# Kernel optimization log

Hardware: AMD Instinct MI355X
Metric: run time of the kernel (lower is better)

## Reference

```python
import jax, jax.numpy as jnp
import numpy as np

H, C = 8, 16           # heads, per-head channels
NEG_SLOPE = 0.2        # PyG GATConv leaky_relu slope
N_NODES, N_EDGES, F_IN, N_GRAPHS = 50000, 600000, 64, 500


def setup_inputs() -> dict:
    key = jax.random.key(0)
    ks = jax.random.split(key, 24)
    s = 0.1  # weight init scale
    inp = {
        "x": jax.random.normal(ks[0], (N_NODES, F_IN), jnp.float32),
        "edge_index": jax.random.randint(ks[1], (2, N_EDGES), 0, N_NODES, dtype=jnp.int64),
        "batch": jnp.sort(jax.random.randint(ks[2], (N_NODES,), 0, N_GRAPHS, dtype=jnp.int64)),
        "W1": jax.random.normal(ks[3], (F_IN, H * C), jnp.float32) * s,
        "as1": jax.random.normal(ks[4], (H, C), jnp.float32) * s,
        "ad1": jax.random.normal(ks[5], (H, C), jnp.float32) * s,
        "b1": jnp.zeros((H * C,), jnp.float32),
        "W2": jax.random.normal(ks[6], (H * C, H * C), jnp.float32) * s,
        "as2": jax.random.normal(ks[7], (H, C), jnp.float32) * s,
        "ad2": jax.random.normal(ks[8], (H, C), jnp.float32) * s,
        "b2": jnp.zeros((H * C,), jnp.float32),
        "W3": jax.random.normal(ks[9], (H * C, H * C), jnp.float32) * s,
        "as3": jax.random.normal(ks[10], (H, C), jnp.float32) * s,
        "ad3": jax.random.normal(ks[11], (H, C), jnp.float32) * s,
        "b3": jnp.zeros((H * C,), jnp.float32),
        "fc1_w": jax.random.normal(ks[12], (H * C, 10), jnp.float32) * s,
        "fc1_b": jnp.zeros((10,), jnp.float32),
        "fc2_w": jax.random.normal(ks[13], (10, 1), jnp.float32) * s,
        "fc2_b": jnp.zeros((1,), jnp.float32),
    }
    return inp


def gat_layer(x, src, dst, W, att_src, att_dst, bias, n):
    # x: [N, F_in] -> h: [N, H, C]
    h = (x @ W).reshape(n, H, C)
    a_src = jnp.sum(h * att_src, axis=-1)  # [N, H]
    a_dst = jnp.sum(h * att_dst, axis=-1)  # [N, H]
    e = jax.nn.leaky_relu(a_src[src] + a_dst[dst], NEG_SLOPE)  # [E, H]
    # per-destination segment softmax (numerically stable)
    m = jax.ops.segment_max(e, dst, num_segments=n)            # [N, H]
    e = jnp.exp(e - m[dst])
    z = jax.ops.segment_sum(e, dst, num_segments=n)            # [N, H]
    alpha = e / (z[dst] + 1e-16)                               # [E, H]
    out = jax.ops.segment_sum(h[src] * alpha[:, :, None], dst, num_segments=n)  # [N, H, C]
    return out.reshape(n, H * C) + bias


def reference(x, edge_index, batch, W1, as1, ad1, b1, W2, as2, ad2, b2,
              W3, as3, ad3, b3, fc1_w, fc1_b, fc2_w, fc2_b):
    n = x.shape[0]
    # PyG GATConv default add_self_loops=True
    loop = jnp.arange(n, dtype=edge_index.dtype)
    src = jnp.concatenate([edge_index[0], loop])
    dst = jnp.concatenate([edge_index[1], loop])

    x = jax.nn.relu(gat_layer(x, src, dst, W1, as1, ad1, b1, n))
    x = jax.nn.relu(gat_layer(x, src, dst, W2, as2, ad2, b2, n))
    x = jax.nn.relu(gat_layer(x, src, dst, W3, as3, ad3, b3, n))

    # global_mean_pool over graphs
    sums = jax.ops.segment_sum(x, batch, num_segments=N_GRAPHS)          # [G, 128]
    cnts = jax.ops.segment_sum(jnp.ones((n,), x.dtype), batch, num_segments=N_GRAPHS)
    pooled = sums / jnp.maximum(cnts, 1.0)[:, None]

    hdn = jax.nn.relu(pooled @ fc1_w + fc1_b)
    return hdn @ fc2_w + fc2_b  # [G, 1]
```

## Files before the change

### kernel.cpp

```cpp
#include <hip/hip_runtime.h>
#include <hip/hip_bf16.h>

#define H 8
#define C 16
#define HC 128
#define NEG_SLOPE 0.2f

__global__ void init_build_kernel(int* __restrict__ zp, int nz,
                                  int* __restrict__ csr, int cap, int sentinel) {
    int i = blockIdx.x * 256 + threadIdx.x;
    if (i < nz) zp[i] = 0;
    if (i < cap) csr[i] = sentinel;
}

__global__ void hist_both_kernel(const int* __restrict__ ei, const int* __restrict__ batch,
                                 int* __restrict__ deg, int* __restrict__ gcnt, int E, int N) {
    int i = blockIdx.x * 256 + threadIdx.x;
    if (i < E + N) {
        int d = (i < E) ? ei[E + i] : i - E;
        atomicAdd(&deg[d], 1);
    }
    if (i < N) atomicAdd(&gcnt[batch[i]], 1);
}

__global__ void scan_blk2_kernel(const int* __restrict__ a1, int* __restrict__ o1,
                                 int* __restrict__ p1, int n1, int nb1, int pad1,
                                 const int* __restrict__ a2, int* __restrict__ o2,
                                 int* __restrict__ p2, int n2, int pad2) {
    __shared__ int sh[256];
    const int* a; int* o; int* p; int n, blk, pad;
    if ((int)blockIdx.x < nb1) { a = a1; o = o1; p = p1; n = n1; blk = blockIdx.x; pad = pad1; }
    else { a = a2; o = o2; p = p2; n = n2; blk = blockIdx.x - nb1; pad = pad2; }
    int tid = threadIdx.x;
    int base = blk * 1024 + tid * 4;
    int4 v = make_int4(0, 0, 0, 0);
    if (base + 3 < n) v = *(const int4*)(a + base);
    else {
        if (base < n)     v.x = a[base];
        if (base + 1 < n) v.y = a[base + 1];
        if (base + 2 < n) v.z = a[base + 2];
        if (base + 3 < n) v.w = a[base + 3];
    }
    if (pad) { v.x = (v.x + 7) & ~7; v.y = (v.y + 7) & ~7; v.z = (v.z + 7) & ~7; v.w = (v.w + 7) & ~7; }
    int s = v.x + v.y + v.z + v.w;
    sh[tid] = s;
    __syncthreads();
    for (int off = 1; off < 256; off <<= 1) {
        int t = (tid >= off) ? sh[tid - off] : 0;
        __syncthreads();
        sh[tid] += t;
        __syncthreads();
    }
    int excl = sh[tid] - s;
    int4 ov;
    ov.x = excl; ov.y = ov.x + v.x; ov.z = ov.y + v.y; ov.w = ov.z + v.z;
    if (base + 3 < n) *(int4*)(o + base) = ov;
    else {
        if (base < n)     o[base] = ov.x;
        if (base + 1 < n) o[base + 1] = ov.y;
        if (base + 2 < n) o[base + 2] = ov.z;
        if (base + 3 < n) o[base + 3] = ov.w;
    }
    if (tid == 255) p[blk] = sh[255];
}

__global__ void scan_part2_kernel(int* __restrict__ p1, int* __restrict__ tot1, int nb1,
                                  int* __restrict__ p2, int* __restrict__ tot2, int nb2) {
    __shared__ int sh[256];
    int tid = threadIdx.x;
    int v = (tid < nb1) ? p1[tid] : 0;
    sh[tid] = v;
    __syncthreads();
    for (int off = 1; off < 256; off <<= 1) {
        int t = (tid >= off) ? sh[tid - off] : 0;
        __syncthreads();
        sh[tid] += t;
        __syncthreads();
    }
    if (tid < nb1) p1[tid] = sh[tid] - v;
    if (tid == 255) *tot1 = sh[255];
    __syncthreads();
    v = (tid < nb2) ? p2[tid] : 0;
    sh[tid] = v;
    __syncthreads();
    for (int off = 1; off < 256; off <<= 1) {
        int t = (tid >= off) ? sh[tid - off] : 0;
        __syncthreads();
        sh[tid] += t;
        __syncthreads();
    }
    if (tid < nb2) p2[tid] = sh[tid] - v;
    if (tid == 255) *tot2 = sh[255];
}

__global__ void scan_add2_kernel(int* __restrict__ o1, const int* __restrict__ p1,
                                 int n1, int nb1,
                                 int* __restrict__ o2, const int* __restrict__ p2, int n2) {
    int* o; const int* p; int n, blk;
    if ((int)blockIdx.x < nb1) { o = o1; p = p1; n = n1; blk = blockIdx.x; }
    else { o = o2; p = p2; n = n2; blk = blockIdx.x - nb1; }
    int off = p[blk];
    int base = blk * 1024 + threadIdx.x * 4;
    if (base + 3 < n) {
        int4 v = *(const int4*)(o + base);
        v.x += off; v.y += off; v.z += off; v.w += off;
        *(int4*)(o + base) = v;
    } else {
        if (base < n)     o[base] += off;
        if (base + 1 < n) o[base + 1] += off;
        if (base + 2 < n) o[base + 2] += off;
        if (base + 3 < n) o[base + 3] += off;
    }
}

__global__ void scatter_kernel(const int* __restrict__ ei, const int* __restrict__ rowptr,
                               int* __restrict__ cursor, int* __restrict__ csr_src,
                               int E, int N) {
    int i = blockIdx.x * 256 + threadIdx.x;
    if (i >= E + N) return;
    int s, d;
    if (i < E) { s = ei[i]; d = ei[E + i]; }
    else       { s = d = i - E; }
    int pos = atomicAdd(&cursor[d], 1);
    csr_src[rowptr[d] + pos] = s;
}

template <int K>
__global__ void gemm_att_kernel(const float* __restrict__ x, const float* __restrict__ W,
                                const float* __restrict__ as_, const float* __restrict__ ad_,
                                float* __restrict__ h, float* __restrict__ asrc,
                                float* __restrict__ adst, int n) {
    const int ROWS = 64;
    __shared__ float xs[ROWS][HC];
    int tx = threadIdx.x & 31;
    int ty = threadIdx.x >> 5;
    int row0 = blockIdx.x * ROWS;

    if (blockIdx.x == 0) {
        if (threadIdx.x < HC) h[(size_t)n * HC + threadIdx.x] = 0.f;
        if (threadIdx.x < H)  asrc[(size_t)n * H + threadIdx.x] = -INFINITY;
    }

    const int NV = ROWS * K / 4;
    for (int idx = threadIdx.x; idx < NV; idx += 256) {
        int rr = idx / (K / 4), kk = idx % (K / 4);
        int gr = row0 + rr;
        float4 v = (gr < n) ? ((const float4*)(x + (size_t)gr * K))[kk]
                            : make_float4(0.f, 0.f, 0.f, 0.f);
        *(float4*)(&xs[rr][kk * 4]) = v;
    }
    __syncthreads();

    const float* Wc = W + tx * 4;
    float acc[8][4];
#pragma unroll
    for (int r = 0; r < 8; ++r)
#pragma unroll
        for (int c = 0; c < 4; ++c) acc[r][c] = 0.f;

    for (int k = 0; k < K; k += 4) {
        float4 wv[4];
#pragma unroll
        for (int kk = 0; kk < 4; ++kk)
            wv[kk] = *(const float4*)(Wc + (size_t)(k + kk) * HC);
#pragma unroll
        for (int r = 0; r < 8; ++r) {
            float4 xr = *(const float4*)(&xs[ty * 8 + r][k]);
            acc[r][0] = fmaf(xr.x, wv[0].x, acc[r][0]);
            acc[r][1] = fmaf(xr.x, wv[0].y, acc[r][1]);
            acc[r][2] = fmaf(xr.x, wv[0].z, acc[r][2]);
            acc[r][3] = fmaf(xr.x, wv[0].w, acc[r][3]);
            acc[r][0] = fmaf(xr.y, wv[1].x, acc[r][0]);
            acc[r][1] = fmaf(xr.y, wv[1].y, acc[r][1]);
            acc[r][2] = fmaf(xr.y, wv[1].z, acc[r][2]);
            acc[r][3] = fmaf(xr.y, wv[1].w, acc[r][3]);
            acc[r][0] = fmaf(xr.z, wv[2].x, acc[r][0]);
            acc[r][1] = fmaf(xr.z, wv[2].y, acc[r][1]);
            acc[r][2] = fmaf(xr.z, wv[2].z, acc[r][2]);
            acc[r][3] = fmaf(xr.z, wv[2].w, acc[r][3]);
            acc[r][0] = fmaf(xr.w, wv[3].x, acc[r][0]);
            acc[r][1] = fmaf(xr.w, wv[3].y, acc[r][1]);
            acc[r][2] = fmaf(xr.w, wv[3].z, acc[r][2]);
            acc[r][3] = fmaf(xr.w, wv[3].w, acc[r][3]);
        }
    }
    __syncthreads();
#pragma unroll
    for (int r = 0; r < 8; ++r) {
        float4 o = make_float4(acc[r][0], acc[r][1], acc[r][2], acc[r][3]);
        *(float4*)(&xs[ty * 8 + r][tx * 4]) = o;
        int row = row0 + ty * 8 + r;
        if (row < n) *(float4*)(h + (size_t)row * HC + tx * 4) = o;
    }
    __syncthreads();

#pragma unroll
    for (int rep = 0; rep < 2; ++rep) {
        int pidx = threadIdx.x + rep * 256;
        int row = pidx >> 3;
        int hd = pidx & 7;
        if (row0 + row < n) {
            const float4* hv = (const float4*)&xs[row][hd * 16];
            const float4* sv = (const float4*)(as_ + hd * 16);
            const float4* dv = (const float4*)(ad_ + hd * 16);
            float s = 0.f, d = 0.f;
#pragma unroll
            for (int j = 0; j < 4; ++j) {
                float4 a = hv[j], u = sv[j], v = dv[j];
                s += a.x * u.x + a.y * u.y + a.z * u.z + a.w * u.w;
                d += a.x * v.x + a.y * v.y + a.z * v.z + a.w * v.w;
            }
            asrc[(size_t)(row0 + row) * H + hd] = s;
            adst[(size_t)(row0 + row) * H + hd] = d;
        }
    }
}

__global__ void gat_agg_kernel(const int* __restrict__ rowptr, const int* __restrict__ csr_src,
                               const float* __restrict__ h, const float* __restrict__ asrc,
                               const float* __restrict__ adst, const float* __restrict__ bias,
                               float* __restrict__ out, int N) {
    int dst = (blockIdx.x * 256 + threadIdx.x) >> 6;
    if (dst >= N) return;
    int lane = threadIdx.x & 63;
    int hd = lane >> 3;
    int beg = rowptr[dst], end = rowptr[dst + 1];
    float ad = adst[(size_t)dst * H + hd];
    const float2* h2 = (const float2*)h;

    float z = 0.f, a0 = 0.f, a1 = 0.f;
    int i0, i1, i2, i3, i4, i5, i6, i7;
    float e0, e1, e2, e3, e4, e5, e6, e7;
    float2 v0, v1, v2, v3, v4, v5, v6, v7;

#define LOADI(S, J) i##S = csr_src[(J)];
#define LOADV(S)                                                           \
    { e##S = asrc[(size_t)i##S * H + hd]; v##S = h2[(size_t)i##S * 64 + lane]; }
#define PROCE(S)                                                           \
    {   float e = e##S + ad;                                               \
        e = e > 0.f ? e : NEG_SLOPE * e;                                   \
        float w = __expf(e);                                               \
        z += w;                                                            \
        a0 = fmaf(w, v##S.x, a0);                                          \
        a1 = fmaf(w, v##S.y, a1);                                          \
    }
    LOADI(0, beg)     LOADI(1, beg + 1) LOADI(2, beg + 2) LOADI(3, beg + 3)
    LOADI(4, beg + 4) LOADI(5, beg + 5) LOADI(6, beg + 6) LOADI(7, beg + 7)
    LOADV(0) LOADV(1) LOADV(2) LOADV(3) LOADV(4) LOADV(5) LOADV(6) LOADV(7)
    LOADI(0, beg + 8)  LOADI(1, beg + 9)  LOADI(2, beg + 10) LOADI(3, beg + 11)
    LOADI(4, beg + 12) LOADI(5, beg + 13) LOADI(6, beg + 14) LOADI(7, beg + 15)

    for (int j = beg; j < end; j += 8) {
        PROCE(0) LOADV(0)
        PROCE(1) LOADV(1)
        PROCE(2) LOADV(2)
        PROCE(3) LOADV(3)
        PROCE(4) LOADV(4)
        PROCE(5) LOADV(5)
        PROCE(6) LOADV(6)
        PROCE(7) LOADV(7)
        LOADI(0, j + 16) LOADI(1, j + 17) LOADI(2, j + 18) LOADI(3, j + 19)
        LOADI(4, j + 20) LOADI(5, j + 21) LOADI(6, j + 22) LOADI(7, j + 23)
    }
#undef LOADI
#undef LOADV
#undef PROCE
    float inv = 1.f / (z + 1e-16f);
    int c2 = lane * 2;
    float r0 = fmaxf(a0 * inv + bias[c2], 0.f);
    float r1 = fmaxf(a1 * inv + bias[c2 + 1], 0.f);
    *(float2*)(out + (size_t)dst * HC + c2) = make_float2(r0, r1);
}

__global__ void pool_mlp_kernel(const float* __restrict__ x, const int* __restrict__ gptr,
                                const float* __restrict__ fc1w, const float* __restrict__ fc1b,
                                const float* __restrict__ fc2w, const float* __restrict__ fc2b,
                                float* __restrict__ out, int G) {
    __shared__ float sp[HC];
    __shared__ float sh[10];
    int g = blockIdx.x;
    int c = threadIdx.x;
    int beg = gptr[g], end = gptr[g + 1];
    float acc = 0.f;
    for (int n = beg; n < end; ++n) acc += x[(size_t)n * HC + c];
    sp[c] = acc / fmaxf((float)(end - beg), 1.f);
    __syncthreads();
    if (c < 10) {
        float s = fc1b[c];
        for (int k = 0; k < HC; ++k) s = fmaf(sp[k], fc1w[k * 10 + c], s);
        sh[c] = fmaxf(s, 0.f);
    }
    __syncthreads();
    if (c == 0) {
        float o = fc2b[0];
#pragma unroll
        for (int j = 0; j < 10; ++j) o = fmaf(sh[j], fc2w[j], o);
        out[g] = o;
    }
}

extern "C" void kernel_launch(void* const* d_in, const int* in_sizes, int n_in,
                              void* d_out, int out_size, void* d_ws, size_t ws_size,
                              hipStream_t stream) {
    const int N = in_sizes[0] / 64;
    const int E = in_sizes[1] / 2;
    const int G = out_size;
    const int ET = E + N;
    const int CSR_CAP = E + 8 * N + 64;

    const float* x     = (const float*)d_in[0];
    const int*   ei    = (const int*)d_in[1];
    const int*   batch = (const int*)d_in[2];
    const float* W1 = (const float*)d_in[3];
    const float* as1 = (const float*)d_in[4];
    const float* ad1 = (const float*)d_in[5];
    const float* b1 = (const float*)d_in[6];
    const float* W2 = (const float*)d_in[7];
    const float* as2 = (const float*)d_in[8];
    const float* ad2 = (const float*)d_in[9];
    const float* b2 = (const float*)d_in[10];
    const float* W3 = (const float*)d_in[11];
    const float* as3 = (const float*)d_in[12];
    const float* ad3 = (const float*)d_in[13];
    const float* b3 = (const float*)d_in[14];
    const float* fc1w = (const float*)d_in[15];
    const float* fc1b = (const float*)d_in[16];
    const float* fc2w = (const float*)d_in[17];
    const float* fc2b = (const float*)d_in[18];

    float* ws = (float*)d_ws;
    float* h    = ws;
    float* xb0  = h + (size_t)(N + 1) * HC;
    float* xb1  = xb0 + (size_t)N * HC;
    float* asrc = xb1 + (size_t)N * HC;
    float* adst = asrc + (size_t)(N + 1) * H;
    int* ints   = (int*)(adst + (size_t)N * H);
    int* deg    = ints;
    int* cursor = deg + N;
    int* gcnt   = cursor + N;
    int* rowptr = gcnt + G;
    int* gptr   = rowptr + N + 16;
    int* partN  = gptr + G + 16;
    int* partG  = partN + 256;
    int* csr    = partG + 256;

    dim3 blk(256);
    int grid_e   = (ET + 255) / 256;
    int grid_agg = (N * 64 + 255) / 256;
    int nbN = (N + 1023) / 1024;
    int nbG = (G + 1023) / 1024;
    int nz = 2 * N + G;
    int grid_init = (max(nz, CSR_CAP) + 255) / 256;

    init_build_kernel<<<grid_init, blk, 0, stream>>>(deg, nz, csr, CSR_CAP, N);
    hist_both_kernel<<<grid_e, blk, 0, stream>>>(ei, batch, deg, gcnt, E, N);
    scan_blk2_kernel<<<nbN + nbG, blk, 0, stream>>>(deg, rowptr, partN, N, nbN, 1,
                                                    gcnt, gptr, partG, G, 0);
    scan_part2_kernel<<<1, blk, 0, stream>>>(partN, rowptr + N, nbN, partG, gptr + G, nbG);
    scan_add2_kernel<<<nbN + nbG, blk, 0, stream>>>(rowptr, partN, N, nbN, gptr, partG, G);
    scatter_kernel<<<grid_e, blk, 0, stream>>>(ei, rowptr, cursor, csr, E, N);

    auto run_layer = [&](const float* xin, int K, const float* W, const float* as_,
                         const float* ad_, const float* b, float* out) {
        if (K == 64)
            gemm_att_kernel<64><<<(N + 63) / 64, blk, 0, stream>>>(xin, W, as_, ad_,
                                                                   h, asrc, adst, N);
        else
            gemm_att_kernel<128><<<(N + 63) / 64, blk, 0, stream>>>(xin, W, as_, ad_,
                                                                    h, asrc, adst, N);
        gat_agg_kernel<<<grid_agg, blk, 0, stream>>>(rowptr, csr, h, asrc, adst, b, out, N);
    };

    run_layer(x,   64,  W1, as1, ad1, b1, xb0);
    run_layer(xb0, 128, W2, as2, ad2, b2, xb1);
    run_layer(xb1, 128, W3, as3, ad3, b3, xb0);

    pool_mlp_kernel<<<G, dim3(128), 0, stream>>>(xb0, gptr, fc1w, fc1b, fc2w, fc2b,
                                                 (float*)d_out, G);
}
```

Baseline: 393.3 us.

## Privatize CSR build atomics into 8 degree copies and derive graph pointers from sorted batch

Splits the destination-degree histogram and scatter cursors into eight per-block-group copies to reduce atomic contention, and processes four edges per thread with vector loads. Self-loops are placed directly at each row start instead of being scattered, and the padding is filled only where needed rather than pre-filling the whole CSR buffer. Graph offsets are computed from boundaries in the sorted batch array instead of a histogram and scan. It adds kernel launches (reduce, base fill) and relies on batch being sorted.

```diff
diff --git a/kernel.cpp b/kernel.cpp
--- a/kernel.cpp
+++ b/kernel.cpp
@@ -6,33 +6,61 @@
 #define HC 128
 #define NEG_SLOPE 0.2f
 
-__global__ void init_build_kernel(int* __restrict__ zp, int nz,
-                                  int* __restrict__ csr, int cap, int sentinel) {
+__global__ void init_kernel(int* __restrict__ deg8, int n) {
     int i = blockIdx.x * 256 + threadIdx.x;
-    if (i < nz) zp[i] = 0;
-    if (i < cap) csr[i] = sentinel;
-}
-
-__global__ void hist_both_kernel(const int* __restrict__ ei, const int* __restrict__ batch,
-                                 int* __restrict__ deg, int* __restrict__ gcnt, int E, int N) {
-    int i = blockIdx.x * 256 + threadIdx.x;
-    if (i < E + N) {
-        int d = (i < E) ? ei[E + i] : i - E;
-        atomicAdd(&deg[d], 1);
-    }
-    if (i < N) atomicAdd(&gcnt[batch[i]], 1);
-}
-
-__global__ void scan_blk2_kernel(const int* __restrict__ a1, int* __restrict__ o1,
-                                 int* __restrict__ p1, int n1, int nb1, int pad1,
-                                 const int* __restrict__ a2, int* __restrict__ o2,
-                                 int* __restrict__ p2, int n2, int pad2) {
+    if (i < n) deg8[i] = 0;
+}
+
+__global__ void hist8_gptr_kernel(const int* __restrict__ ei, const int* __restrict__ batch,
+                                  int* __restrict__ deg8, int* __restrict__ gptr,
+                                  int E, int N, int G) {
+    int t = blockIdx.x * 256 + threadIdx.x;
+    int* dg = deg8 + (size_t)(blockIdx.x & 7) * N;
+    int e0 = t * 4;
+    if (e0 + 3 < E) {
+        int4 d4 = *(const int4*)(ei + E + e0);
+        atomicAdd(&dg[d4.x], 1);
+        atomicAdd(&dg[d4.y], 1);
+        atomicAdd(&dg[d4.z], 1);
+        atomicAdd(&dg[d4.w], 1);
+    } else if (e0 < E) {
+        for (int j = e0; j < E; ++j) atomicAdd(&dg[ei[E + j]], 1);
+    }
+    int n0 = t * 4;
+    if (n0 < N) {
+        int v0 = batch[n0];
+        int v1 = (n0 + 1 < N) ? batch[n0 + 1] : v0;
+        int v2 = (n0 + 2 < N) ? batch[n0 + 2] : v1;
+        int v3 = (n0 + 3 < N) ? batch[n0 + 3] : v2;
+        int vals[4] = {v0, v1, v2, v3};
+        int prev = (n0 == 0) ? -1 : batch[n0 - 1];
+        for (int j = 0; j < 4; ++j) {
+            int i = n0 + j;
+            if (i >= N) break;
+            int cur = vals[j];
+            if (cur != prev)
+                for (int g = prev + 1; g <= cur; ++g) gptr[g] = i;
+            if (i == N - 1)
+                for (int g = cur + 1; g <= G; ++g) gptr[g] = N;
+            prev = cur;
+        }
+    }
+}
+
+__global__ void deg_reduce_kernel(const int* __restrict__ deg8, int* __restrict__ deg, int N) {
+    int d = blockIdx.x * 256 + threadIdx.x;
+    if (d >= N) return;
+    int s = 1;
+#pragma unroll
+    for (int c = 0; c < 8; ++c) s += deg8[(size_t)c * N + d];
+    deg[d] = s;
+}
+
+__global__ void scan_blk_kernel(const int* __restrict__ a, int* __restrict__ o,
+                                int* __restrict__ p, int n) {
     __shared__ int sh[256];
-    const int* a; int* o; int* p; int n, blk, pad;
-    if ((int)blockIdx.x < nb1) { a = a1; o = o1; p = p1; n = n1; blk = blockIdx.x; pad = pad1; }
-    else { a = a2; o = o2; p = p2; n = n2; blk = blockIdx.x - nb1; pad = pad2; }
     int tid = threadIdx.x;
-    int base = blk * 1024 + tid * 4;
+    int base = blockIdx.x * 1024 + tid * 4;
     int4 v = make_int4(0, 0, 0, 0);
     if (base + 3 < n) v = *(const int4*)(a + base);
     else {
@@ -41,7 +69,11 @@
         if (base + 2 < n) v.z = a[base + 2];
         if (base + 3 < n) v.w = a[base + 3];
     }
-    if (pad) { v.x = (v.x + 7) & ~7; v.y = (v.y + 7) & ~7; v.z = (v.z + 7) & ~7; v.w = (v.w + 7) & ~7; }
+    v.x = (v.x + 7) & ~7; v.y = (v.y + 7) & ~7; v.z = (v.z + 7) & ~7; v.w = (v.w + 7) & ~7;
+    if (base >= n)     v.x = 0;
+    if (base + 1 >= n) v.y = 0;
+    if (base + 2 >= n) v.z = 0;
+    if (base + 3 >= n) v.w = 0;
     int s = v.x + v.y + v.z + v.w;
     sh[tid] = s;
     __syncthreads();
@@ -61,14 +93,13 @@
         if (base + 2 < n) o[base + 2] = ov.z;
         if (base + 3 < n) o[base + 3] = ov.w;
     }
-    if (tid == 255) p[blk] = sh[255];
-}
-
-__global__ void scan_part2_kernel(int* __restrict__ p1, int* __restrict__ tot1, int nb1,
-                                  int* __restrict__ p2, int* __restrict__ tot2, int nb2) {
+    if (tid == 255) p[blockIdx.x] = sh[255];
+}
+
+__global__ void scan_part_kernel(int* __restrict__ p, int* __restrict__ tot, int nb) {
     __shared__ int sh[256];
     int tid = threadIdx.x;
-    int v = (tid < nb1) ? p1[tid] : 0;
+    int v = (tid < nb) ? p[tid] : 0;
     sh[tid] = v;
     __syncthreads();
     for (int off = 1; off < 256; off <<= 1) {
@@ -77,30 +108,13 @@
         sh[tid] += t;
         __syncthreads();
     }
-    if (tid < nb1) p1[tid] = sh[tid] - v;
-    if (tid == 255) *tot1 = sh[255];
-    __syncthreads();
-    v = (tid < nb2) ? p2[tid] : 0;
-    sh[tid] = v;
-    __syncthreads();
-    for (int off = 1; off < 256; off <<= 1) {
-        int t = (tid >= off) ? sh[tid - off] : 0;
-        __syncthreads();
-        sh[tid] += t;
-        __syncthreads();
-    }
-    if (tid < nb2) p2[tid] = sh[tid] - v;
-    if (tid == 255) *tot2 = sh[255];
-}
-
-__global__ void scan_add2_kernel(int* __restrict__ o1, const int* __restrict__ p1,
-                                 int n1, int nb1,
-                                 int* __restrict__ o2, const int* __restrict__ p2, int n2) {
-    int* o; const int* p; int n, blk;
-    if ((int)blockIdx.x < nb1) { o = o1; p = p1; n = n1; blk = blockIdx.x; }
-    else { o = o2; p = p2; n = n2; blk = blockIdx.x - nb1; }
-    int off = p[blk];
-    int base = blk * 1024 + threadIdx.x * 4;
+    if (tid < nb) p[tid] = sh[tid] - v;
+    if (tid == 255) *tot = sh[255];
+}
+
+__global__ void scan_add_kernel(int* __restrict__ o, const int* __restrict__ p, int n) {
+    int off = p[blockIdx.x];
+    int base = blockIdx.x * 1024 + threadIdx.x * 4;
     if (base + 3 < n) {
         int4 v = *(const int4*)(o + base);
         v.x += off; v.y += off; v.z += off; v.w += off;
@@ -113,16 +127,45 @@
     }
 }
 
-__global__ void scatter_kernel(const int* __restrict__ ei, const int* __restrict__ rowptr,
-                               int* __restrict__ cursor, int* __restrict__ csr_src,
-                               int E, int N) {
-    int i = blockIdx.x * 256 + threadIdx.x;
-    if (i >= E + N) return;
-    int s, d;
-    if (i < E) { s = ei[i]; d = ei[E + i]; }
-    else       { s = d = i - E; }
-    int pos = atomicAdd(&cursor[d], 1);
-    csr_src[rowptr[d] + pos] = s;
+__global__ void base_fill_kernel(int* __restrict__ deg8 ,
+                                 const int* __restrict__ rowptr, int* __restrict__ csr, int N) {
+    int d = blockIdx.x * 256 + threadIdx.x;
+    if (d >= N) return;
+    int base = rowptr[d];
+    csr[base] = d;
+    int run = base + 1;
+    int cnt[8];
+#pragma unroll
+    for (int c = 0; c < 8; ++c) cnt[c] = deg8[(size_t)c * N + d];
+#pragma unroll
+    for (int c = 0; c < 8; ++c) { deg8[(size_t)c * N + d] = run; run += cnt[c]; }
+    int rend = rowptr[d + 1];
+    for (int p = run; p < rend; ++p) csr[p] = N;
+    if (d == 0) {
+        int tot = rowptr[N];
+        for (int k = 0; k < 64; ++k) csr[tot + k] = N;
+    }
+}
+
+__global__ void scatter8_kernel(const int* __restrict__ ei, int* __restrict__ base8,
+                                int* __restrict__ csr, int E, int N) {
+    int t = blockIdx.x * 256 + threadIdx.x;
+    int* cur = base8 + (size_t)(blockIdx.x & 7) * N;
+    int e0 = t * 4;
+    if (e0 + 3 < E) {
+        int4 s4 = *(const int4*)(ei + e0);
+        int4 d4 = *(const int4*)(ei + E + e0);
+        int p;
+        p = atomicAdd(&cur[d4.x], 1); csr[p] = s4.x;
+        p = atomicAdd(&cur[d4.y], 1); csr[p] = s4.y;
+        p = atomicAdd(&cur[d4.z], 1); csr[p] = s4.z;
+        p = atomicAdd(&cur[d4.w], 1); csr[p] = s4.w;
+    } else if (e0 < E) {
+        for (int j = e0; j < E; ++j) {
+            int p = atomicAdd(&cur[ei[E + j]], 1);
+            csr[p] = ei[j];
+        }
+    }
 }
 
 template <int K>
@@ -305,7 +348,6 @@
     const int N = in_sizes[0] / 64;
     const int E = in_sizes[1] / 2;
     const int G = out_size;
-    const int ET = E + N;
     const int CSR_CAP = E + 8 * N + 64;
 
     const float* x     = (const float*)d_in[0];
@@ -335,30 +377,27 @@
     float* asrc = xb1 + (size_t)N * HC;
     float* adst = asrc + (size_t)(N + 1) * H;
     int* ints   = (int*)(adst + (size_t)N * H);
-    int* deg    = ints;
-    int* cursor = deg + N;
-    int* gcnt   = cursor + N;
-    int* rowptr = gcnt + G;
+    int* deg8   = ints;
+    int* deg    = deg8 + (size_t)8 * N;
+    int* rowptr = deg + N;
     int* gptr   = rowptr + N + 16;
     int* partN  = gptr + G + 16;
-    int* partG  = partN + 256;
-    int* csr    = partG + 256;
+    int* csr    = partN + 256;
 
     dim3 blk(256);
-    int grid_e   = (ET + 255) / 256;
+    int grid4   = ((E + 3) / 4 + 255) / 256;
+    int grid_n  = (N + 255) / 256;
     int grid_agg = (N * 64 + 255) / 256;
     int nbN = (N + 1023) / 1024;
-    int nbG = (G + 1023) / 1024;
-    int nz = 2 * N + G;
-    int grid_init = (max(nz, CSR_CAP) + 255) / 256;
-
-    init_build_kernel<<<grid_init, blk, 0, stream>>>(deg, nz, csr, CSR_CAP, N);
-    hist_both_kernel<<<grid_e, blk, 0, stream>>>(ei, batch, deg, gcnt, E, N);
-    scan_blk2_kernel<<<nbN + nbG, blk, 0, stream>>>(deg, rowptr, partN, N, nbN, 1,
-                                                    gcnt, gptr, partG, G, 0);
-    scan_part2_kernel<<<1, blk, 0, stream>>>(partN, rowptr + N, nbN, partG, gptr + G, nbG);
-    scan_add2_kernel<<<nbN + nbG, blk, 0, stream>>>(rowptr, partN, N, nbN, gptr, partG, G);
-    scatter_kernel<<<grid_e, blk, 0, stream>>>(ei, rowptr, cursor, csr, E, N);
+
+    init_kernel<<<(8 * N + 255) / 256, blk, 0, stream>>>(deg8, 8 * N);
+    hist8_gptr_kernel<<<grid4, blk, 0, stream>>>(ei, batch, deg8, gptr, E, N, G);
+    deg_reduce_kernel<<<grid_n, blk, 0, stream>>>(deg8, deg, N);
+    scan_blk_kernel<<<nbN, blk, 0, stream>>>(deg, rowptr, partN, N);
+    scan_part_kernel<<<1, blk, 0, stream>>>(partN, rowptr + N, nbN);
+    scan_add_kernel<<<nbN, blk, 0, stream>>>(rowptr, partN, N);
+    base_fill_kernel<<<grid_n, blk, 0, stream>>>(deg8, rowptr, csr, N);
+    scatter8_kernel<<<grid4, blk, 0, stream>>>(ei, deg8, csr, E, N);
 
     auto run_layer = [&](const float* xin, int K, const float* W, const float* as_,
                          const float* ad_, const float* b, float* out) {
```

Result: faster. 366.0 us (-6.9%).
